# Optimization experiments

Measured on AMD Instinct MI355X. Metric: run time of the kernel, lower is better.

Reference implementation:

```python
import jax, jax.numpy as jnp
import numpy as np

DECAY = 0.99
EPS = 1e-05


def setup_inputs() -> dict:
    key = jax.random.key(0)
    k1, k2, k3, k4 = jax.random.split(key, 4)
    x = jax.random.normal(k1, (32, 64, 64, 64), jnp.float32)          # [B,H,W,dim]
    embed = jax.random.normal(k2, (64, 1024), jnp.float32)            # [dim, n_embed] buffer
    cluster_size = jax.random.uniform(k3, (1024,), jnp.float32)       # EMA cluster-size buffer
    embed_avg = jax.random.normal(k4, (64, 1024), jnp.float32)        # EMA embed-avg buffer
    return {"x": x, "embed": embed, "cluster_size": cluster_size, "embed_avg": embed_avg}


def reference(x, embed, cluster_size, embed_avg):
    dim = x.shape[-1]
    n_embed = embed.shape[1]
    flatten = x.reshape(-1, dim)                                      # [N, dim]
    # squared distances: ||f||^2 - 2 f.E + ||e||^2   -> [N, n_embed]
    dist = ((flatten * flatten).sum(1, keepdims=True)
            - 2.0 * (flatten @ embed)
            + (embed * embed).sum(0, keepdims=True))
    idx = jnp.argmin(dist, axis=1)                                    # [N]
    quantize = jnp.take(embed.T, idx, axis=0).reshape(x.shape)        # codebook gather
    embed_ind = idx.reshape(x.shape[:-1])

    # EMA codebook update (training branch); stats detached as in torch (buffers, .data ops)
    fl = jax.lax.stop_gradient(flatten)
    onehot_sum = jax.ops.segment_sum(jnp.ones_like(idx, dtype=x.dtype), idx, num_segments=n_embed)
    embed_sum = jax.ops.segment_sum(fl, idx, num_segments=n_embed).T  # [dim, n_embed]
    new_cluster_size = DECAY * cluster_size + (1.0 - DECAY) * onehot_sum
    new_embed_avg = DECAY * embed_avg + (1.0 - DECAY) * embed_sum
    n = new_cluster_size.sum()
    cs = (new_cluster_size + EPS) / (n + n_embed * EPS) * n
    new_embed = new_embed_avg / cs[None, :]

    diff = jnp.mean((jax.lax.stop_gradient(quantize) - x) ** 2)       # commitment loss
    quantize_st = x + jax.lax.stop_gradient(quantize - x)             # straight-through
    return (quantize_st, diff, embed_ind, new_cluster_size, new_embed_avg, new_embed)
```

## Files before the change

### kernel.cpp

```cpp
#include <hip/hip_runtime.h>


#define N_ROWS 131072
#define DIM    64
#define NEMB   1024
#define FLAG_CAP 131072
#define TAU 0.02f
#define NRANGE 32

static constexpr float DECAYF = 0.99f;
static constexpr float OMDF   = (float)(1.0 - 0.99);
static constexpr float EPSF   = 1e-5f;
static constexpr float NEPSF  = (float)(1024 * 1e-5);

typedef __attribute__((ext_vector_type(8))) short short8;
typedef __attribute__((ext_vector_type(4))) float f32x4;

static __device__ __forceinline__ unsigned short f2bf(float f) {
    unsigned int u = __builtin_bit_cast(unsigned int, f);
    unsigned int r = (u + 0x7FFFu + ((u >> 16) & 1u)) >> 16;
    return (unsigned short)r;
}
static __device__ __forceinline__ float bf2f(unsigned short h) {
    unsigned int u = ((unsigned int)h) << 16;
    return __builtin_bit_cast(float, u);
}

#define WS_ESUM    0
#define WS_CNTF    65536
#define WS_DIFF    66560
#define WS_FLAGCNT 66561
#define WS_N       66562
#define WS_EE      66564
#define WS_EMBEDT  67588
#define WS_IDX     133124
#define WS_FLAGLST 264196
#define WS_BFRAG   395268
#define WS_CNTPART 460804
#define WS_PART    493572
#define WS_NEED_BYTES ((size_t)(WS_PART + NRANGE * 65536) * 4)

__global__ void prep_kernel(const float* __restrict__ embed,
                            float* __restrict__ embedT,
                            float* __restrict__ ee,
                            uint4* __restrict__ BfragG) {
    int tid = blockIdx.x * 256 + threadIdx.x;
    for (int i = 0; i < 4; ++i) {
        int id = i * 16384 + tid;
        int d = id >> 10, e = id & 1023;
        embedT[e * 64 + d] = embed[id];
    }
    if (tid < NEMB) {
        float s = 0.f;
        for (int d = 0; d < DIM; ++d) {
            float v = embed[d * 1024 + tid];
            s = fmaf(v, v, s);
        }
        ee[tid] = s;
    }
    int fid  = tid >> 6;
    int lane = tid & 63;
    int hl = fid & 1, kt = (fid >> 1) & 1, ct = fid >> 2;
    int col = ct * 16 + (lane & 15);
    int k0  = kt * 32 + (lane >> 4) * 8;
    unsigned short u[8];
    #pragma unroll
    for (int j = 0; j < 8; ++j) {
        float v = -2.0f * embed[(k0 + j) * 1024 + col];
        unsigned short h = f2bf(v);
        if (hl) h = f2bf(v - bf2f(h));
        u[j] = h;
    }
    uint4 wv;
    wv.x = (unsigned)u[0] | ((unsigned)u[1] << 16);
    wv.y = (unsigned)u[2] | ((unsigned)u[3] << 16);
    wv.z = (unsigned)u[4] | ((unsigned)u[5] << 16);
    wv.w = (unsigned)u[6] | ((unsigned)u[7] << 16);
    BfragG[fid * 64 + lane] = wv;
}

__global__ __launch_bounds__(256) void dist_kernel(
        const float* __restrict__ x, const uint4* __restrict__ BfragG,
        const float* __restrict__ ee, const float* __restrict__ embedT,
        float* __restrict__ out_q, float* __restrict__ out_ind,
        int* __restrict__ ws_idx, float* __restrict__ ws_diff,
        int* __restrict__ ws_flagcnt, int* __restrict__ ws_flaglist) {
    __shared__ float sEE[1024];
    __shared__ int   sIdx[64];
    __shared__ float red[4];

    const int t = threadIdx.x;
    const int w = t >> 6, lane = t & 63;
    const int quad = lane >> 4, wl = lane & 15;
    const int rbase = blockIdx.x * 64;

    short8 a_hi[2], a_lo[2];
    {
        int row = rbase + w * 16 + wl;
        #pragma unroll
        for (int kt = 0; kt < 2; ++kt) {
            const float* px = x + (size_t)row * 64 + kt * 32 + quad * 8;
            float4 v0 = *(const float4*)px;
            float4 v1 = *(const float4*)(px + 4);
            float vv[8] = {v0.x, v0.y, v0.z, v0.w, v1.x, v1.y, v1.z, v1.w};
            short8 ah, al;
            #pragma unroll
            for (int j = 0; j < 8; ++j) {
                unsigned short h = f2bf(vv[j]);
                ah[j] = (short)h;
                al[j] = (short)f2bf(vv[j] - bf2f(h));
            }
            a_hi[kt] = ah; a_lo[kt] = al;
        }
    }

    for (int i = t; i < 1024; i += 256) sEE[i] = ee[i];

    float b1[4], b2[4];
    int   i1[4];
    #pragma unroll
    for (int s = 0; s < 4; ++s) { b1[s] = 3.4e38f; b2[s] = 3.4e38f; i1[s] = 0; }

    const f32x4 zacc = {0.f, 0.f, 0.f, 0.f};

    __syncthreads();

    const uint4* bg = BfragG + lane;
    uint4 nb0 = bg[0], nb1 = bg[64], nb2 = bg[128], nb3 = bg[192];
    for (int g = 0; g < 64; ++g) {
        uint4 c_b0 = nb0, c_b1 = nb1, c_b2 = nb2, c_b3 = nb3;
        if (g < 63) {
            const uint4* p = bg + (g + 1) * 256;
            nb0 = p[0]; nb1 = p[64]; nb2 = p[128]; nb3 = p[192];
        }
        short8 bh0 = __builtin_bit_cast(short8, c_b0);
        short8 bl0 = __builtin_bit_cast(short8, c_b1);
        short8 bh1 = __builtin_bit_cast(short8, c_b2);
        short8 bl1 = __builtin_bit_cast(short8, c_b3);
        int col = g * 16 + wl;
        float eec = sEE[col];
        {
            f32x4 c0 = __builtin_amdgcn_mfma_f32_16x16x32_bf16(a_lo[0], bh0, zacc, 0, 0, 0);
            f32x4 c1 = __builtin_amdgcn_mfma_f32_16x16x32_bf16(a_lo[1], bh1, zacc, 0, 0, 0);
            c0 = __builtin_amdgcn_mfma_f32_16x16x32_bf16(a_hi[0], bl0, c0, 0, 0, 0);
            c1 = __builtin_amdgcn_mfma_f32_16x16x32_bf16(a_hi[1], bl1, c1, 0, 0, 0);
            c0 = __builtin_amdgcn_mfma_f32_16x16x32_bf16(a_hi[0], bh0, c0, 0, 0, 0);
            c1 = __builtin_amdgcn_mfma_f32_16x16x32_bf16(a_hi[1], bh1, c1, 0, 0, 0);
            #pragma unroll
            for (int reg = 0; reg < 4; ++reg) {
                float s = c0[reg] + c1[reg] + eec;
                bool lt = s < b1[reg];
                b2[reg] = fminf(fmaxf(s, b1[reg]), b2[reg]);
                i1[reg] = lt ? col : i1[reg];
                b1[reg] = fminf(s, b1[reg]);
            }
        }
    }

    for (int m = 1; m < 16; m <<= 1) {
        #pragma unroll
        for (int s = 0; s < 4; ++s) {
            float ob1 = __shfl_xor(b1[s], m);
            int   oi1 = __shfl_xor(i1[s], m);
            float ob2 = __shfl_xor(b2[s], m);
            if (ob1 < b1[s] || (ob1 == b1[s] && oi1 < i1[s])) {
                b2[s] = fminf(b1[s], ob2); b1[s] = ob1; i1[s] = oi1;
            } else {
                b2[s] = fminf(b2[s], ob1);
            }
        }
    }
    if (wl == 0) {
        #pragma unroll
        for (int s = 0; s < 4; ++s) {
            int rloc = w * 16 + quad * 4 + s;
            int row = rbase + rloc;
            sIdx[rloc] = i1[s];
            ws_idx[row] = i1[s];
            out_ind[row] = (float)i1[s];
            if (b2[s] - b1[s] < TAU) {
                int pos = atomicAdd(ws_flagcnt, 1);
                if (pos < FLAG_CAP) ws_flaglist[pos] = row;
            }
        }
    }
    __syncthreads();

    {
        int r = t >> 2, hh = t & 3;
        int e = sIdx[r];
        const float4* et = (const float4*)(embedT + e * 64 + hh * 16);
        const float4* xr = (const float4*)(x + (size_t)(rbase + r) * 64 + hh * 16);
        float4*       qo = (float4*)(out_q + (size_t)(rbase + r) * 64 + hh * 16);
        float dsum = 0.f;
        #pragma unroll
        for (int v = 0; v < 4; ++v) {
            float4 q4 = et[v];
            float4 x4 = xr[v];
            float dx = q4.x - x4.x, dy = q4.y - x4.y, dz = q4.z - x4.z, dw = q4.w - x4.w;
            float4 o;
            o.x = x4.x + dx; o.y = x4.y + dy; o.z = x4.z + dz; o.w = x4.w + dw;
            qo[v] = o;
            dsum += dx * dx + dy * dy + dz * dz + dw * dw;
        }
        for (int o2 = 32; o2 > 0; o2 >>= 1) dsum += __shfl_down(dsum, o2);
        if (lane == 0) red[w] = dsum;
        __syncthreads();
        if (t == 0) atomicAdd(ws_diff, red[0] + red[1] + red[2] + red[3]);
    }
}

__global__ __launch_bounds__(256) void recheck_kernel(
        const float* __restrict__ x, const float* __restrict__ embed,
        const float* __restrict__ embedT, const float* __restrict__ ee,
        const int* __restrict__ flagcnt, const int* __restrict__ flaglist,
        int* __restrict__ ws_idx, float* __restrict__ out_ind,
        float* __restrict__ out_q, float* __restrict__ ws_diff) {
    __shared__ float sx[8][64];
    __shared__ float sff[8];
    __shared__ int   srow[8];
    __shared__ float sbd[8][256];
    __shared__ int   sbi[8][256];
    const int t = threadIdx.x;
    const int w = t >> 6, lane = t & 63;
    int cnt = *flagcnt;
    if (cnt > FLAG_CAP) cnt = FLAG_CAP;
    int ntiles = (cnt + 7) >> 3;
    for (int tile = blockIdx.x; tile < ntiles; tile += gridDim.x) {
        int base = tile * 8;
        int nr = cnt - base; if (nr > 8) nr = 8;
        __syncthreads();
        if (t < nr) srow[t] = flaglist[base + t];
        __syncthreads();
        for (int l = t; l < nr * 64; l += 256)
            sx[l >> 6][l & 63] = x[(size_t)srow[l >> 6] * 64 + (l & 63)];
        __syncthreads();
        if (t < nr) {
            float ff = 0.f;
            for (int k = 0; k < 64; ++k) ff = fmaf(sx[t][k], sx[t][k], ff);
            sff[t] = ff;
        }
        float acc[8][4];
        #pragma unroll
        for (int r = 0; r < 8; ++r)
            #pragma unroll
            for (int j = 0; j < 4; ++j) acc[r][j] = 0.f;
        int c0 = t * 4;
        for (int k = 0; k < 64; ++k) {
            float4 e4 = *(const float4*)(embed + k * 1024 + c0);
            #pragma unroll
            for (int r = 0; r < 8; ++r) {
                float xk = sx[r][k];
                acc[r][0] = fmaf(xk, e4.x, acc[r][0]);
                acc[r][1] = fmaf(xk, e4.y, acc[r][1]);
                acc[r][2] = fmaf(xk, e4.z, acc[r][2]);
                acc[r][3] = fmaf(xk, e4.w, acc[r][3]);
            }
        }
        __syncthreads();
        #pragma unroll
        for (int r = 0; r < 8; ++r) {
            float ff = sff[r];
            float bd = 3.4e38f; int bi = 0;
            #pragma unroll
            for (int j = 0; j < 4; ++j) {
                float d = (ff - 2.f * acc[r][j]) + ee[c0 + j];
                if (d < bd) { bd = d; bi = c0 + j; }
            }
            sbd[r][t] = bd; sbi[r][t] = bi;
        }
        __syncthreads();
        #pragma unroll
        for (int rr = 0; rr < 2; ++rr) {
            int r = w * 2 + rr;
            if (r < nr) {
                float bd = sbd[r][lane]; int bi = sbi[r][lane];
                #pragma unroll
                for (int k2 = 1; k2 < 4; ++k2) {
                    float od = sbd[r][lane + 64 * k2];
                    int   oi = sbi[r][lane + 64 * k2];
                    if (od < bd || (od == bd && oi < bi)) { bd = od; bi = oi; }
                }
                for (int m = 32; m > 0; m >>= 1) {
                    float od = __shfl_xor(bd, m);
                    int   oi = __shfl_xor(bi, m);
                    if (od < bd || (od == bd && oi < bi)) { bd = od; bi = oi; }
                }
                int row = srow[r];
                int oi_old = ws_idx[row];
                if (bi != oi_old) {
                    float xv = sx[r][lane];
                    float dn   = embedT[bi * 64 + lane] - xv;
                    float dold = embedT[oi_old * 64 + lane] - xv;
                    out_q[(size_t)row * 64 + lane] = xv + dn;
                    float delta = dn * dn - dold * dold;
                    for (int o = 32; o > 0; o >>= 1) delta += __shfl_down(delta, o);
                    if (lane == 0) {
                        ws_idx[row] = bi;
                        out_ind[row] = (float)bi;
                        atomicAdd(ws_diff, delta);
                    }
                }
            }
        }
    }
}

__global__ __launch_bounds__(1024) void scatter_kernel(
        const int* __restrict__ idx, const float* __restrict__ x,
        float* __restrict__ part_or_esum, float* __restrict__ cntp_or_cntf,
        int use_atomic) {
    __shared__ float shist[8192];
    __shared__ float scnt[1024];
    const int t = threadIdx.x;
    const int bid = blockIdx.x;
    const int oct = (bid >> 3) & 7;
    const int rb  = (bid & 7) | ((bid >> 6) << 3);
    const int sid = rb * 8 + oct;
    const int w = t >> 6, lane = t & 63;
    const int g = lane >> 3, d = lane & 7;

    for (int i = t; i < 8192; i += 1024) shist[i] = 0.f;
    if (oct == 0) { if (t < 1024) scnt[t] = 0.f; }
    __syncthreads();

    const int row0 = rb * 4096 + w * 256;
    int rcur = row0 + g;
    int e_n = idx[rcur];
    float x_n = x[(size_t)rcur * 64 + oct * 8 + d];
    for (int it = 0; it < 32; ++it) {
        int e = e_n; float xv = x_n;
        int rnext = rcur + 8;
        if (it < 31) {
            e_n = idx[rnext];
            x_n = x[(size_t)rnext * 64 + oct * 8 + d];
        }
        rcur = rnext;
        atomicAdd(&shist[e * 8 + d], xv);
        if (oct == 0 && d == 0) atomicAdd(&scnt[e], 1.0f);
    }
    __syncthreads();

    if (!use_atomic) {
        float* dst = part_or_esum + (size_t)sid * 8192;
        for (int out = t; out < 8192; out += 1024)
            dst[out] = shist[(out & 1023) * 8 + (out >> 10)];
        if (oct == 0) {
            float* cdst = cntp_or_cntf + rb * 1024;
            if (t < 1024) cdst[t] = scnt[t];
        }
    } else {
        for (int out = t; out < 8192; out += 1024) {
            float v = shist[(out & 1023) * 8 + (out >> 10)];
            if (v != 0.f)
                atomicAdd(&part_or_esum[(oct * 8 + (out >> 10)) * 1024 + (out & 1023)], v);
        }
        if (oct == 0) {
            if (t < 1024) {
                float c = scnt[t];
                if (c != 0.f) atomicAdd(&cntp_or_cntf[t], c);
            }
        }
    }
}

__global__ __launch_bounds__(1024) void finalize1(
        const float* __restrict__ cluster_size, const float* __restrict__ cntp,
        int nrb, const float* __restrict__ ws_diff, float* __restrict__ out_diff,
        float* __restrict__ out_ncs, float* __restrict__ ws_n) {
    int t = threadIdx.x;
    float c = 0.f;
    for (int k = 0; k < nrb; ++k) c += cntp[k * 1024 + t];
    float ncs = DECAYF * cluster_size[t] + OMDF * c;
    out_ncs[t] = ncs;
    __shared__ float sred[16];
    float v = ncs;
    for (int o = 32; o > 0; o >>= 1) v += __shfl_down(v, o);
    if ((t & 63) == 0) sred[t >> 6] = v;
    __syncthreads();
    if (t == 0) {
        float n = 0.f;
        for (int i = 0; i < 16; ++i) n += sred[i];
        ws_n[0] = n;
        out_diff[0] = ws_diff[0] * (1.0f / 8388608.0f);
    }
}

__global__ __launch_bounds__(256) void finalize2(
        const float* __restrict__ embed_avg, const float* __restrict__ part,
        int nrb, const float* __restrict__ out_ncs, const float* __restrict__ ws_n,
        float* __restrict__ out_nea, float* __restrict__ out_ne) {
    int j = blockIdx.x * 256 + threadIdx.x;
    float es = 0.f;
    for (int k = 0; k < nrb; ++k) es += part[(size_t)k * 65536 + j];
    float n = ws_n[0];
    float nea = DECAYF * embed_avg[j] + OMDF * es;
    out_nea[j] = nea;
    float ncs = out_ncs[j & 1023];
    float cs = (ncs + EPSF) / (n + NEPSF) * n;
    out_ne[j] = nea / cs;
}

extern "C" void kernel_launch(void* const* d_in, const int* in_sizes, int n_in,
                              void* d_out, int out_size, void* d_ws, size_t ws_size,
                              hipStream_t stream) {
    const float* x            = (const float*)d_in[0];
    const float* embed        = (const float*)d_in[1];
    const float* cluster_size = (const float*)d_in[2];
    const float* embed_avg    = (const float*)d_in[3];

    float* out = (float*)d_out;
    float* out_q    = out;
    float* out_diff = out + 8388608;
    float* out_ind  = out + 8388609;
    float* out_ncs  = out + 8519681;
    float* out_nea  = out + 8520705;
    float* out_ne   = out + 8586241;

    float* ws = (float*)d_ws;
    float* ws_esum     = ws + WS_ESUM;
    float* ws_cntf     = ws + WS_CNTF;
    float* ws_diff     = ws + WS_DIFF;
    int*   ws_flagcnt  = (int*)(ws + WS_FLAGCNT);
    float* ws_n        = ws + WS_N;
    float* ws_ee       = ws + WS_EE;
    float* ws_embedT   = ws + WS_EMBEDT;
    int*   ws_idx      = (int*)(ws + WS_IDX);
    int*   ws_flaglist = (int*)(ws + WS_FLAGLST);
    uint4* ws_Bfrag    = (uint4*)(ws + WS_BFRAG);
    float* ws_cntpart  = ws + WS_CNTPART;
    float* ws_part     = ws + WS_PART;

    const int use_part = (ws_size >= WS_NEED_BYTES) ? 1 : 0;

    if (use_part) {
        hipMemsetAsync(ws + WS_DIFF, 0, 8, stream);
    } else {
        hipMemsetAsync(d_ws, 0, (size_t)(WS_FLAGCNT + 1) * 4, stream);
    }

    prep_kernel<<<64, 256, 0, stream>>>(embed, ws_embedT, ws_ee, ws_Bfrag);
    dist_kernel<<<N_ROWS / 64, 256, 0, stream>>>(x, ws_Bfrag, ws_ee, ws_embedT,
                                                 out_q, out_ind, ws_idx, ws_diff,
                                                 ws_flagcnt, ws_flaglist);
    recheck_kernel<<<1024, 256, 0, stream>>>(x, embed, ws_embedT, ws_ee,
                                             ws_flagcnt, ws_flaglist,
                                             ws_idx, out_ind, out_q, ws_diff);
    scatter_kernel<<<NRANGE * 8, 1024, 0, stream>>>(
        ws_idx, x,
        use_part ? ws_part : ws_esum,
        use_part ? ws_cntpart : ws_cntf,
        use_part ? 0 : 1);
    finalize1<<<1, 1024, 0, stream>>>(cluster_size,
                                      use_part ? ws_cntpart : ws_cntf,
                                      use_part ? NRANGE : 1,
                                      ws_diff, out_diff, out_ncs, ws_n);
    finalize2<<<256, 256, 0, stream>>>(embed_avg,
                                       use_part ? ws_part : ws_esum,
                                       use_part ? NRANGE : 1,
                                       out_ncs, ws_n, out_nea, out_ne);
}
```

Before: 305.3 us.

## Process four row tiles per wave to reuse codebook fragments across rows

Each wave of the distance kernel now handles 64 rows (four 16-row MFMA tiles) instead of 16, so every codebook B-fragment loaded from global memory feeds four times as many MFMAs. The grid shrinks by four, and blocks start the codebook sweep at a staggered group offset to spread cache traffic. The second-best tracking uses a single med3 instruction, and the recheck kernel handles 16 flagged rows per tile instead of 8. The cost is much higher register pressure (16 tracked rows, 16 A fragments per lane), which may lower occupancy, and only 512 blocks remain to fill the GPU.

```diff
diff --git a/kernel.cpp b/kernel.cpp
--- a/kernel.cpp
+++ b/kernel.cpp
@@ -86,17 +86,18 @@
         int* __restrict__ ws_idx, float* __restrict__ ws_diff,
         int* __restrict__ ws_flagcnt, int* __restrict__ ws_flaglist) {
     __shared__ float sEE[1024];
-    __shared__ int   sIdx[64];
+    __shared__ int   sIdx[256];
     __shared__ float red[4];
 
     const int t = threadIdx.x;
     const int w = t >> 6, lane = t & 63;
     const int quad = lane >> 4, wl = lane & 15;
-    const int rbase = blockIdx.x * 64;
-
-    short8 a_hi[2], a_lo[2];
-    {
-        int row = rbase + w * 16 + wl;
+    const int rbase = blockIdx.x * 256;
+
+    short8 a_hi[4][2], a_lo[4][2];
+    #pragma unroll
+    for (int rt = 0; rt < 4; ++rt) {
+        int row = rbase + w * 64 + rt * 16 + wl;
         #pragma unroll
         for (int kt = 0; kt < 2; ++kt) {
             const float* px = x + (size_t)row * 64 + kt * 32 + quad * 8;
@@ -110,56 +111,63 @@
                 ah[j] = (short)h;
                 al[j] = (short)f2bf(vv[j] - bf2f(h));
             }
-            a_hi[kt] = ah; a_lo[kt] = al;
+            a_hi[rt][kt] = ah; a_lo[rt][kt] = al;
         }
     }
 
     for (int i = t; i < 1024; i += 256) sEE[i] = ee[i];
 
-    float b1[4], b2[4];
-    int   i1[4];
+    float b1[16], b2[16];
+    int   i1[16];
     #pragma unroll
-    for (int s = 0; s < 4; ++s) { b1[s] = 3.4e38f; b2[s] = 3.4e38f; i1[s] = 0; }
+    for (int s = 0; s < 16; ++s) { b1[s] = 3.4e38f; b2[s] = 3.4e38f; i1[s] = 0; }
 
     const f32x4 zacc = {0.f, 0.f, 0.f, 0.f};
 
     __syncthreads();
 
-    const uint4* bg = BfragG + lane;
-    uint4 nb0 = bg[0], nb1 = bg[64], nb2 = bg[128], nb3 = bg[192];
+    const int goff = blockIdx.x & 63;
+    int gv = goff;
+    {
+    }
+    const uint4* p0 = BfragG + gv * 256 + lane;
+    uint4 nb0 = p0[0], nb1 = p0[64], nb2 = p0[128], nb3 = p0[192];
     for (int g = 0; g < 64; ++g) {
         uint4 c_b0 = nb0, c_b1 = nb1, c_b2 = nb2, c_b3 = nb3;
+        const int col = gv * 16 + wl;
         if (g < 63) {
-            const uint4* p = bg + (g + 1) * 256;
+            gv = (gv + 1) & 63;
+            const uint4* p = BfragG + gv * 256 + lane;
             nb0 = p[0]; nb1 = p[64]; nb2 = p[128]; nb3 = p[192];
         }
         short8 bh0 = __builtin_bit_cast(short8, c_b0);
         short8 bl0 = __builtin_bit_cast(short8, c_b1);
         short8 bh1 = __builtin_bit_cast(short8, c_b2);
         short8 bl1 = __builtin_bit_cast(short8, c_b3);
-        int col = g * 16 + wl;
         float eec = sEE[col];
-        {
-            f32x4 c0 = __builtin_amdgcn_mfma_f32_16x16x32_bf16(a_lo[0], bh0, zacc, 0, 0, 0);
-            f32x4 c1 = __builtin_amdgcn_mfma_f32_16x16x32_bf16(a_lo[1], bh1, zacc, 0, 0, 0);
-            c0 = __builtin_amdgcn_mfma_f32_16x16x32_bf16(a_hi[0], bl0, c0, 0, 0, 0);
-            c1 = __builtin_amdgcn_mfma_f32_16x16x32_bf16(a_hi[1], bl1, c1, 0, 0, 0);
-            c0 = __builtin_amdgcn_mfma_f32_16x16x32_bf16(a_hi[0], bh0, c0, 0, 0, 0);
-            c1 = __builtin_amdgcn_mfma_f32_16x16x32_bf16(a_hi[1], bh1, c1, 0, 0, 0);
+        #pragma unroll
+        for (int rt = 0; rt < 4; ++rt) {
+            f32x4 c0 = __builtin_amdgcn_mfma_f32_16x16x32_bf16(a_lo[rt][0], bh0, zacc, 0, 0, 0);
+            f32x4 c1 = __builtin_amdgcn_mfma_f32_16x16x32_bf16(a_lo[rt][1], bh1, zacc, 0, 0, 0);
+            c0 = __builtin_amdgcn_mfma_f32_16x16x32_bf16(a_hi[rt][0], bl0, c0, 0, 0, 0);
+            c1 = __builtin_amdgcn_mfma_f32_16x16x32_bf16(a_hi[rt][1], bl1, c1, 0, 0, 0);
+            c0 = __builtin_amdgcn_mfma_f32_16x16x32_bf16(a_hi[rt][0], bh0, c0, 0, 0, 0);
+            c1 = __builtin_amdgcn_mfma_f32_16x16x32_bf16(a_hi[rt][1], bh1, c1, 0, 0, 0);
             #pragma unroll
             for (int reg = 0; reg < 4; ++reg) {
                 float s = c0[reg] + c1[reg] + eec;
-                bool lt = s < b1[reg];
-                b2[reg] = fminf(fmaxf(s, b1[reg]), b2[reg]);
-                i1[reg] = lt ? col : i1[reg];
-                b1[reg] = fminf(s, b1[reg]);
+                int st = rt * 4 + reg;
+                bool lt = s < b1[st];
+                b2[st] = __builtin_amdgcn_fmed3f(s, b1[st], b2[st]);
+                i1[st] = lt ? col : i1[st];
+                b1[st] = fminf(s, b1[st]);
             }
         }
     }
 
     for (int m = 1; m < 16; m <<= 1) {
         #pragma unroll
-        for (int s = 0; s < 4; ++s) {
+        for (int s = 0; s < 16; ++s) {
             float ob1 = __shfl_xor(b1[s], m);
             int   oi1 = __shfl_xor(i1[s], m);
             float ob2 = __shfl_xor(b2[s], m);
@@ -172,8 +180,9 @@
     }
     if (wl == 0) {
         #pragma unroll
-        for (int s = 0; s < 4; ++s) {
-            int rloc = w * 16 + quad * 4 + s;
+        for (int s = 0; s < 16; ++s) {
+            int rt = s >> 2, reg = s & 3;
+            int rloc = w * 64 + rt * 16 + quad * 4 + reg;
             int row = rbase + rloc;
             sIdx[rloc] = i1[s];
             ws_idx[row] = i1[s];
@@ -187,21 +196,24 @@
     __syncthreads();
 
     {
-        int r = t >> 2, hh = t & 3;
-        int e = sIdx[r];
-        const float4* et = (const float4*)(embedT + e * 64 + hh * 16);
-        const float4* xr = (const float4*)(x + (size_t)(rbase + r) * 64 + hh * 16);
-        float4*       qo = (float4*)(out_q + (size_t)(rbase + r) * 64 + hh * 16);
         float dsum = 0.f;
         #pragma unroll
-        for (int v = 0; v < 4; ++v) {
-            float4 q4 = et[v];
-            float4 x4 = xr[v];
-            float dx = q4.x - x4.x, dy = q4.y - x4.y, dz = q4.z - x4.z, dw = q4.w - x4.w;
-            float4 o;
-            o.x = x4.x + dx; o.y = x4.y + dy; o.z = x4.z + dz; o.w = x4.w + dw;
-            qo[v] = o;
-            dsum += dx * dx + dy * dy + dz * dz + dw * dw;
+        for (int half = 0; half < 2; ++half) {
+            int r = half * 128 + (t >> 1), hh = t & 1;
+            int e = sIdx[r];
+            const float4* et = (const float4*)(embedT + e * 64 + hh * 32);
+            const float4* xr = (const float4*)(x + (size_t)(rbase + r) * 64 + hh * 32);
+            float4*       qo = (float4*)(out_q + (size_t)(rbase + r) * 64 + hh * 32);
+            #pragma unroll
+            for (int v = 0; v < 8; ++v) {
+                float4 q4 = et[v];
+                float4 x4 = xr[v];
+                float dx = q4.x - x4.x, dy = q4.y - x4.y, dz = q4.z - x4.z, dw = q4.w - x4.w;
+                float4 o;
+                o.x = x4.x + dx; o.y = x4.y + dy; o.z = x4.z + dz; o.w = x4.w + dw;
+                qo[v] = o;
+                dsum += dx * dx + dy * dy + dz * dz + dw * dw;
+            }
         }
         for (int o2 = 32; o2 > 0; o2 >>= 1) dsum += __shfl_down(dsum, o2);
         if (lane == 0) red[w] = dsum;
@@ -216,19 +228,19 @@
         const int* __restrict__ flagcnt, const int* __restrict__ flaglist,
         int* __restrict__ ws_idx, float* __restrict__ out_ind,
         float* __restrict__ out_q, float* __restrict__ ws_diff) {
-    __shared__ float sx[8][64];
-    __shared__ float sff[8];
-    __shared__ int   srow[8];
-    __shared__ float sbd[8][256];
-    __shared__ int   sbi[8][256];
+    __shared__ float sx[16][64];
+    __shared__ float sff[16];
+    __shared__ int   srow[16];
+    __shared__ float sbd[16][256];
+    __shared__ int   sbi[16][256];
     const int t = threadIdx.x;
     const int w = t >> 6, lane = t & 63;
     int cnt = *flagcnt;
     if (cnt > FLAG_CAP) cnt = FLAG_CAP;
-    int ntiles = (cnt + 7) >> 3;
+    int ntiles = (cnt + 15) >> 4;
     for (int tile = blockIdx.x; tile < ntiles; tile += gridDim.x) {
-        int base = tile * 8;
-        int nr = cnt - base; if (nr > 8) nr = 8;
+        int base = tile * 16;
+        int nr = cnt - base; if (nr > 16) nr = 16;
         __syncthreads();
         if (t < nr) srow[t] = flaglist[base + t];
         __syncthreads();
@@ -240,16 +252,16 @@
             for (int k = 0; k < 64; ++k) ff = fmaf(sx[t][k], sx[t][k], ff);
             sff[t] = ff;
         }
-        float acc[8][4];
-        #pragma unroll
-        for (int r = 0; r < 8; ++r)
+        float acc[16][4];
+        #pragma unroll
+        for (int r = 0; r < 16; ++r)
             #pragma unroll
             for (int j = 0; j < 4; ++j) acc[r][j] = 0.f;
         int c0 = t * 4;
         for (int k = 0; k < 64; ++k) {
             float4 e4 = *(const float4*)(embed + k * 1024 + c0);
             #pragma unroll
-            for (int r = 0; r < 8; ++r) {
+            for (int r = 0; r < 16; ++r) {
                 float xk = sx[r][k];
                 acc[r][0] = fmaf(xk, e4.x, acc[r][0]);
                 acc[r][1] = fmaf(xk, e4.y, acc[r][1]);
@@ -259,20 +271,22 @@
         }
         __syncthreads();
         #pragma unroll
-        for (int r = 0; r < 8; ++r) {
-            float ff = sff[r];
-            float bd = 3.4e38f; int bi = 0;
-            #pragma unroll
-            for (int j = 0; j < 4; ++j) {
-                float d = (ff - 2.f * acc[r][j]) + ee[c0 + j];
-                if (d < bd) { bd = d; bi = c0 + j; }
-            }
-            sbd[r][t] = bd; sbi[r][t] = bi;
-        }
-        __syncthreads();
-        #pragma unroll
-        for (int rr = 0; rr < 2; ++rr) {
-            int r = w * 2 + rr;
+        for (int r = 0; r < 16; ++r) {
+            if (r < nr) {
+                float ff = sff[r];
+                float bd = 3.4e38f; int bi = 0;
+                #pragma unroll
+                for (int j = 0; j < 4; ++j) {
+                    float d = (ff - 2.f * acc[r][j]) + ee[c0 + j];
+                    if (d < bd) { bd = d; bi = c0 + j; }
+                }
+                sbd[r][t] = bd; sbi[r][t] = bi;
+            }
+        }
+        __syncthreads();
+        #pragma unroll
+        for (int rr = 0; rr < 4; ++rr) {
+            int r = w * 4 + rr;
             if (r < nr) {
                 float bd = sbd[r][lane]; int bi = sbi[r][lane];
                 #pragma unroll
@@ -440,9 +454,9 @@
     }
 
     prep_kernel<<<64, 256, 0, stream>>>(embed, ws_embedT, ws_ee, ws_Bfrag);
-    dist_kernel<<<N_ROWS / 64, 256, 0, stream>>>(x, ws_Bfrag, ws_ee, ws_embedT,
-                                                 out_q, out_ind, ws_idx, ws_diff,
-                                                 ws_flagcnt, ws_flaglist);
+    dist_kernel<<<N_ROWS / 256, 256, 0, stream>>>(x, ws_Bfrag, ws_ee, ws_embedT,
+                                                  out_q, out_ind, ws_idx, ws_diff,
+                                                  ws_flagcnt, ws_flaglist);
     recheck_kernel<<<1024, 256, 0, stream>>>(x, embed, ws_embedT, ws_ee,
                                              ws_flagcnt, ws_flaglist,
                                              ws_idx, out_ind, out_q, ws_diff);
```

Measured after the change: 268.3 us. -12.1%, faster.

## Fuse recheck into dist kernel, pack index into distance key, merge finalizers

Applied to the files above, without the earlier changes.

The distance kernel now handles 128 rows per block with two row tiles that share each codebook fragment load. It packs the codebook index into the low mantissa bits of the distance, so top-2 tracking becomes fmin/fmed3 with no index select. Near-tie rows are queued in shared memory and re-scored exactly in fp32 inside the same kernel, which removes the separate recheck launch and the global flag atomics. The two finalize kernels are merged into one, and the memset is replaced by a zero write in prep. Truncating the mantissa lowers key precision, so the tie threshold is widened to compensate, which can send more rows through the slow exact path. Each block also starts at a different codebook offset to spread the fragment reads.

```diff
diff --git a/kernel.cpp b/kernel.cpp
--- a/kernel.cpp
+++ b/kernel.cpp
@@ -4,9 +4,9 @@
 #define N_ROWS 131072
 #define DIM    64
 #define NEMB   1024
-#define FLAG_CAP 131072
-#define TAU 0.02f
 #define NRANGE 32
+#define KMASK  0xFFFFFC00u
+#define TAUK   0.15f
 
 static constexpr float DECAYF = 0.99f;
 static constexpr float OMDF   = (float)(1.0 - 0.99);
@@ -43,8 +43,10 @@
 __global__ void prep_kernel(const float* __restrict__ embed,
                             float* __restrict__ embedT,
                             float* __restrict__ ee,
-                            uint4* __restrict__ BfragG) {
+                            uint4* __restrict__ BfragG,
+                            float* __restrict__ ws_diff) {
     int tid = blockIdx.x * 256 + threadIdx.x;
+    if (tid == 0) ws_diff[0] = 0.f;
     for (int i = 0; i < 4; ++i) {
         int id = i * 16384 + tid;
         int d = id >> 10, e = id & 1023;
@@ -81,22 +83,30 @@
 
 __global__ __launch_bounds__(256) void dist_kernel(
         const float* __restrict__ x, const uint4* __restrict__ BfragG,
-        const float* __restrict__ ee, const float* __restrict__ embedT,
+        const float* __restrict__ ee, const float* __restrict__ embed,
+        const float* __restrict__ embedT,
         float* __restrict__ out_q, float* __restrict__ out_ind,
-        int* __restrict__ ws_idx, float* __restrict__ ws_diff,
-        int* __restrict__ ws_flagcnt, int* __restrict__ ws_flaglist) {
+        int* __restrict__ ws_idx, float* __restrict__ ws_diff) {
     __shared__ float sEE[1024];
-    __shared__ int   sIdx[64];
+    __shared__ int   sIdx[128];
     __shared__ float red[4];
+    __shared__ int   sFlagCnt;
+    __shared__ int   sFlagRows[128];
+    __shared__ float sx[8][64];
+    __shared__ float sff[8];
+    __shared__ float sbdw[8][4];
+    __shared__ int   sbiw[8][4];
+    __shared__ int   schg[8];
 
     const int t = threadIdx.x;
     const int w = t >> 6, lane = t & 63;
     const int quad = lane >> 4, wl = lane & 15;
-    const int rbase = blockIdx.x * 64;
-
-    short8 a_hi[2], a_lo[2];
-    {
-        int row = rbase + w * 16 + wl;
+    const int rbase = blockIdx.x * 128;
+
+    short8 a_hi[2][2], a_lo[2][2];
+    #pragma unroll
+    for (int rt = 0; rt < 2; ++rt) {
+        int row = rbase + w * 32 + rt * 16 + wl;
         #pragma unroll
         for (int kt = 0; kt < 2; ++kt) {
             const float* px = x + (size_t)row * 64 + kt * 32 + quad * 8;
@@ -110,91 +120,115 @@
                 ah[j] = (short)h;
                 al[j] = (short)f2bf(vv[j] - bf2f(h));
             }
-            a_hi[kt] = ah; a_lo[kt] = al;
+            a_hi[rt][kt] = ah; a_lo[rt][kt] = al;
         }
     }
 
     for (int i = t; i < 1024; i += 256) sEE[i] = ee[i];
-
-    float b1[4], b2[4];
-    int   i1[4];
+    if (t == 0) sFlagCnt = 0;
+
+    float b1[8], b2[8];
     #pragma unroll
-    for (int s = 0; s < 4; ++s) { b1[s] = 3.4e38f; b2[s] = 3.4e38f; i1[s] = 0; }
+    for (int s = 0; s < 8; ++s) { b1[s] = 3.4e38f; b2[s] = 3.4e38f; }
 
     const f32x4 zacc = {0.f, 0.f, 0.f, 0.f};
 
     __syncthreads();
 
-    const uint4* bg = BfragG + lane;
-    uint4 nb0 = bg[0], nb1 = bg[64], nb2 = bg[128], nb3 = bg[192];
-    for (int g = 0; g < 64; ++g) {
-        uint4 c_b0 = nb0, c_b1 = nb1, c_b2 = nb2, c_b3 = nb3;
-        if (g < 63) {
-            const uint4* p = bg + (g + 1) * 256;
-            nb0 = p[0]; nb1 = p[64]; nb2 = p[128]; nb3 = p[192];
-        }
-        short8 bh0 = __builtin_bit_cast(short8, c_b0);
-        short8 bl0 = __builtin_bit_cast(short8, c_b1);
-        short8 bh1 = __builtin_bit_cast(short8, c_b2);
-        short8 bl1 = __builtin_bit_cast(short8, c_b3);
-        int col = g * 16 + wl;
-        float eec = sEE[col];
-        {
-            f32x4 c0 = __builtin_amdgcn_mfma_f32_16x16x32_bf16(a_lo[0], bh0, zacc, 0, 0, 0);
-            f32x4 c1 = __builtin_amdgcn_mfma_f32_16x16x32_bf16(a_lo[1], bh1, zacc, 0, 0, 0);
-            c0 = __builtin_amdgcn_mfma_f32_16x16x32_bf16(a_hi[0], bl0, c0, 0, 0, 0);
-            c1 = __builtin_amdgcn_mfma_f32_16x16x32_bf16(a_hi[1], bl1, c1, 0, 0, 0);
-            c0 = __builtin_amdgcn_mfma_f32_16x16x32_bf16(a_hi[0], bh0, c0, 0, 0, 0);
-            c1 = __builtin_amdgcn_mfma_f32_16x16x32_bf16(a_hi[1], bh1, c1, 0, 0, 0);
-            #pragma unroll
-            for (int reg = 0; reg < 4; ++reg) {
-                float s = c0[reg] + c1[reg] + eec;
-                bool lt = s < b1[reg];
-                b2[reg] = fminf(fmaxf(s, b1[reg]), b2[reg]);
-                i1[reg] = lt ? col : i1[reg];
-                b1[reg] = fminf(s, b1[reg]);
-            }
-        }
-    }
+    const int goff = blockIdx.x & 63;
+
+#define GBODY(CB0, CB1, CB2, CB3, COLV)                                        \
+    {                                                                          \
+        short8 bh0 = __builtin_bit_cast(short8, CB0);                          \
+        short8 bl0 = __builtin_bit_cast(short8, CB1);                          \
+        short8 bh1 = __builtin_bit_cast(short8, CB2);                          \
+        short8 bl1 = __builtin_bit_cast(short8, CB3);                          \
+        float eec = sEE[COLV];                                                 \
+        unsigned colu = (unsigned)(COLV);                                      \
+        _Pragma("unroll")                                                      \
+        for (int rt = 0; rt < 2; ++rt) {                                       \
+            f32x4 c0 = __builtin_amdgcn_mfma_f32_16x16x32_bf16(a_lo[rt][0], bh0, zacc, 0, 0, 0); \
+            f32x4 c1 = __builtin_amdgcn_mfma_f32_16x16x32_bf16(a_lo[rt][1], bh1, zacc, 0, 0, 0); \
+            c0 = __builtin_amdgcn_mfma_f32_16x16x32_bf16(a_hi[rt][0], bl0, c0, 0, 0, 0); \
+            c1 = __builtin_amdgcn_mfma_f32_16x16x32_bf16(a_hi[rt][1], bl1, c1, 0, 0, 0); \
+            c0 = __builtin_amdgcn_mfma_f32_16x16x32_bf16(a_hi[rt][0], bh0, c0, 0, 0, 0); \
+            c1 = __builtin_amdgcn_mfma_f32_16x16x32_bf16(a_hi[rt][1], bh1, c1, 0, 0, 0); \
+            _Pragma("unroll")                                                  \
+            for (int reg = 0; reg < 4; ++reg) {                                \
+                float s = c0[reg] + c1[reg] + eec;                             \
+                unsigned ku = (__builtin_bit_cast(unsigned, s) & KMASK) | colu;\
+                float key = __builtin_bit_cast(float, ku);                     \
+                int st = rt * 4 + reg;                                         \
+                b2[st] = __builtin_amdgcn_fmed3f(key, b1[st], b2[st]);         \
+                b1[st] = fminf(key, b1[st]);                                   \
+            }                                                                  \
+        }                                                                      \
+    }
+
+    {
+        const uint4* bgl = BfragG + lane;
+        int gA = goff, gB = (goff + 1) & 63;
+        const uint4* pA = bgl + gA * 256;
+        uint4 A0 = pA[0], A1 = pA[64], A2 = pA[128], A3 = pA[192];
+        const uint4* pB = bgl + gB * 256;
+        uint4 B0 = pB[0], B1 = pB[64], B2 = pB[128], B3 = pB[192];
+        for (int it = 0; it < 64; it += 2) {
+            int colA = ((goff + it) & 63) * 16 + wl;
+            GBODY(A0, A1, A2, A3, colA);
+            if (it + 2 < 64) {
+                const uint4* p = bgl + (((goff + it + 2) & 63) * 256);
+                A0 = p[0]; A1 = p[64]; A2 = p[128]; A3 = p[192];
+            }
+            int colB = ((goff + it + 1) & 63) * 16 + wl;
+            GBODY(B0, B1, B2, B3, colB);
+            if (it + 3 < 64) {
+                const uint4* p = bgl + (((goff + it + 3) & 63) * 256);
+                B0 = p[0]; B1 = p[64]; B2 = p[128]; B3 = p[192];
+            }
+        }
+    }
+#undef GBODY
 
     for (int m = 1; m < 16; m <<= 1) {
         #pragma unroll
-        for (int s = 0; s < 4; ++s) {
-            float ob1 = __shfl_xor(b1[s], m);
-            int   oi1 = __shfl_xor(i1[s], m);
-            float ob2 = __shfl_xor(b2[s], m);
-            if (ob1 < b1[s] || (ob1 == b1[s] && oi1 < i1[s])) {
-                b2[s] = fminf(b1[s], ob2); b1[s] = ob1; i1[s] = oi1;
-            } else {
-                b2[s] = fminf(b2[s], ob1);
-            }
+        for (int s = 0; s < 8; ++s) {
+            float o1 = __shfl_xor(b1[s], m);
+            float o2 = __shfl_xor(b2[s], m);
+            float mx = fmaxf(b1[s], o1);
+            b1[s] = fminf(b1[s], o1);
+            b2[s] = fminf(fminf(b2[s], o2), mx);
         }
     }
     if (wl == 0) {
         #pragma unroll
-        for (int s = 0; s < 4; ++s) {
-            int rloc = w * 16 + quad * 4 + s;
+        for (int s = 0; s < 8; ++s) {
+            int rt = s >> 2, reg = s & 3;
+            int rloc = w * 32 + rt * 16 + quad * 4 + reg;
             int row = rbase + rloc;
-            sIdx[rloc] = i1[s];
-            ws_idx[row] = i1[s];
-            out_ind[row] = (float)i1[s];
-            if (b2[s] - b1[s] < TAU) {
-                int pos = atomicAdd(ws_flagcnt, 1);
-                if (pos < FLAG_CAP) ws_flaglist[pos] = row;
+            unsigned kb = __builtin_bit_cast(unsigned, b1[s]);
+            int col = (int)(kb & 1023u);
+            sIdx[rloc] = col;
+            ws_idx[row] = col;
+            out_ind[row] = (float)col;
+            float v1 = __builtin_bit_cast(float, kb & KMASK);
+            float v2 = __builtin_bit_cast(float, __builtin_bit_cast(unsigned, b2[s]) & KMASK);
+            if (v2 - v1 < TAUK) {
+                int p = atomicAdd(&sFlagCnt, 1);
+                sFlagRows[p] = rloc;
             }
         }
     }
     __syncthreads();
 
     {
-        int r = t >> 2, hh = t & 3;
+        int r = t >> 1, hh = t & 1;
         int e = sIdx[r];
-        const float4* et = (const float4*)(embedT + e * 64 + hh * 16);
-        const float4* xr = (const float4*)(x + (size_t)(rbase + r) * 64 + hh * 16);
-        float4*       qo = (float4*)(out_q + (size_t)(rbase + r) * 64 + hh * 16);
+        const float4* et = (const float4*)(embedT + e * 64 + hh * 32);
+        const float4* xr = (const float4*)(x + (size_t)(rbase + r) * 64 + hh * 32);
+        float4*       qo = (float4*)(out_q + (size_t)(rbase + r) * 64 + hh * 32);
         float dsum = 0.f;
         #pragma unroll
-        for (int v = 0; v < 4; ++v) {
+        for (int v = 0; v < 8; ++v) {
             float4 q4 = et[v];
             float4 x4 = xr[v];
             float dx = q4.x - x4.x, dy = q4.y - x4.y, dz = q4.z - x4.z, dw = q4.w - x4.w;
@@ -208,32 +242,16 @@
         __syncthreads();
         if (t == 0) atomicAdd(ws_diff, red[0] + red[1] + red[2] + red[3]);
     }
-}
-
-__global__ __launch_bounds__(256) void recheck_kernel(
-        const float* __restrict__ x, const float* __restrict__ embed,
-        const float* __restrict__ embedT, const float* __restrict__ ee,
-        const int* __restrict__ flagcnt, const int* __restrict__ flaglist,
-        int* __restrict__ ws_idx, float* __restrict__ out_ind,
-        float* __restrict__ out_q, float* __restrict__ ws_diff) {
-    __shared__ float sx[8][64];
-    __shared__ float sff[8];
-    __shared__ int   srow[8];
-    __shared__ float sbd[8][256];
-    __shared__ int   sbi[8][256];
-    const int t = threadIdx.x;
-    const int w = t >> 6, lane = t & 63;
-    int cnt = *flagcnt;
-    if (cnt > FLAG_CAP) cnt = FLAG_CAP;
-    int ntiles = (cnt + 7) >> 3;
-    for (int tile = blockIdx.x; tile < ntiles; tile += gridDim.x) {
-        int base = tile * 8;
-        int nr = cnt - base; if (nr > 8) nr = 8;
-        __syncthreads();
-        if (t < nr) srow[t] = flaglist[base + t];
-        __syncthreads();
-        for (int l = t; l < nr * 64; l += 256)
-            sx[l >> 6][l & 63] = x[(size_t)srow[l >> 6] * 64 + (l & 63)];
+
+    __syncthreads();
+    int fcnt = sFlagCnt;
+    for (int base = 0; base < fcnt; base += 8) {
+        int nr = fcnt - base; if (nr > 8) nr = 8;
+        __syncthreads();
+        for (int l = t; l < nr * 64; l += 256) {
+            int rl = sFlagRows[base + (l >> 6)];
+            sx[l >> 6][l & 63] = x[(size_t)(rbase + rl) * 64 + (l & 63)];
+        }
         __syncthreads();
         if (t < nr) {
             float ff = 0.f;
@@ -245,9 +263,9 @@
         for (int r = 0; r < 8; ++r)
             #pragma unroll
             for (int j = 0; j < 4; ++j) acc[r][j] = 0.f;
-        int c0 = t * 4;
+        int c0i = t * 4;
         for (int k = 0; k < 64; ++k) {
-            float4 e4 = *(const float4*)(embed + k * 1024 + c0);
+            float4 e4 = *(const float4*)(embed + k * 1024 + c0i);
             #pragma unroll
             for (int r = 0; r < 8; ++r) {
                 float xk = sx[r][k];
@@ -260,47 +278,52 @@
         __syncthreads();
         #pragma unroll
         for (int r = 0; r < 8; ++r) {
-            float ff = sff[r];
-            float bd = 3.4e38f; int bi = 0;
-            #pragma unroll
-            for (int j = 0; j < 4; ++j) {
-                float d = (ff - 2.f * acc[r][j]) + ee[c0 + j];
-                if (d < bd) { bd = d; bi = c0 + j; }
-            }
-            sbd[r][t] = bd; sbi[r][t] = bi;
-        }
-        __syncthreads();
-        #pragma unroll
-        for (int rr = 0; rr < 2; ++rr) {
-            int r = w * 2 + rr;
             if (r < nr) {
-                float bd = sbd[r][lane]; int bi = sbi[r][lane];
+                float ff = sff[r];
+                float bd = 3.4e38f; int bi = 0;
                 #pragma unroll
-                for (int k2 = 1; k2 < 4; ++k2) {
-                    float od = sbd[r][lane + 64 * k2];
-                    int   oi = sbi[r][lane + 64 * k2];
-                    if (od < bd || (od == bd && oi < bi)) { bd = od; bi = oi; }
+                for (int j = 0; j < 4; ++j) {
+                    float d = (ff - 2.f * acc[r][j]) + sEE[c0i + j];
+                    if (d < bd) { bd = d; bi = c0i + j; }
                 }
                 for (int m = 32; m > 0; m >>= 1) {
                     float od = __shfl_xor(bd, m);
                     int   oi = __shfl_xor(bi, m);
                     if (od < bd || (od == bd && oi < bi)) { bd = od; bi = oi; }
                 }
-                int row = srow[r];
-                int oi_old = ws_idx[row];
-                if (bi != oi_old) {
-                    float xv = sx[r][lane];
-                    float dn   = embedT[bi * 64 + lane] - xv;
-                    float dold = embedT[oi_old * 64 + lane] - xv;
-                    out_q[(size_t)row * 64 + lane] = xv + dn;
-                    float delta = dn * dn - dold * dold;
-                    for (int o = 32; o > 0; o >>= 1) delta += __shfl_down(delta, o);
-                    if (lane == 0) {
-                        ws_idx[row] = bi;
-                        out_ind[row] = (float)bi;
-                        atomicAdd(ws_diff, delta);
-                    }
-                }
+                if (lane == 0) { sbdw[r][w] = bd; sbiw[r][w] = bi; }
+            }
+        }
+        __syncthreads();
+        if (t < nr) {
+            float bd = sbdw[t][0]; int bi = sbiw[t][0];
+            #pragma unroll
+            for (int k2 = 1; k2 < 4; ++k2) {
+                float od = sbdw[t][k2]; int oi = sbiw[t][k2];
+                if (od < bd || (od == bd && oi < bi)) { bd = od; bi = oi; }
+            }
+            int rl = sFlagRows[base + t];
+            int oi_ = sIdx[rl];
+            schg[t] = (bi != oi_) ? bi : -1;
+            if (bi != oi_) {
+                ws_idx[rbase + rl] = bi;
+                out_ind[rbase + rl] = (float)bi;
+            }
+        }
+        __syncthreads();
+        for (int r = w; r < nr; r += 4) {
+            int ni = schg[r];
+            if (ni >= 0) {
+                int rl = sFlagRows[base + r];
+                int row = rbase + rl;
+                int oi_ = sIdx[rl];
+                float xv = sx[r][lane];
+                float dn   = embedT[ni * 64 + lane] - xv;
+                float dold = embedT[oi_ * 64 + lane] - xv;
+                out_q[(size_t)row * 64 + lane] = xv + dn;
+                float delta = dn * dn - dold * dold;
+                for (int o = 32; o > 0; o >>= 1) delta += __shfl_down(delta, o);
+                if (lane == 0) atomicAdd(ws_diff, delta);
             }
         }
     }
@@ -364,39 +387,37 @@
     }
 }
 
-__global__ __launch_bounds__(1024) void finalize1(
+__global__ __launch_bounds__(1024) void finalizeF(
         const float* __restrict__ cluster_size, const float* __restrict__ cntp,
-        int nrb, const float* __restrict__ ws_diff, float* __restrict__ out_diff,
-        float* __restrict__ out_ncs, float* __restrict__ ws_n) {
-    int t = threadIdx.x;
+        const float* __restrict__ part, int nrb,
+        const float* __restrict__ ws_diff, const float* __restrict__ embed_avg,
+        float* __restrict__ out_diff, float* __restrict__ out_ncs,
+        float* __restrict__ out_nea, float* __restrict__ out_ne) {
+    __shared__ float sred[16];
+    __shared__ float sn;
+    const int tid = threadIdx.x;
+    const int b = blockIdx.x;
     float c = 0.f;
-    for (int k = 0; k < nrb; ++k) c += cntp[k * 1024 + t];
-    float ncs = DECAYF * cluster_size[t] + OMDF * c;
-    out_ncs[t] = ncs;
-    __shared__ float sred[16];
+    for (int k = 0; k < nrb; ++k) c += cntp[k * 1024 + tid];
+    float ncs = DECAYF * cluster_size[tid] + OMDF * c;
     float v = ncs;
     for (int o = 32; o > 0; o >>= 1) v += __shfl_down(v, o);
-    if ((t & 63) == 0) sred[t >> 6] = v;
-    __syncthreads();
-    if (t == 0) {
+    if ((tid & 63) == 0) sred[tid >> 6] = v;
+    __syncthreads();
+    if (tid == 0) {
         float n = 0.f;
         for (int i = 0; i < 16; ++i) n += sred[i];
-        ws_n[0] = n;
-        out_diff[0] = ws_diff[0] * (1.0f / 8388608.0f);
-    }
-}
-
-__global__ __launch_bounds__(256) void finalize2(
-        const float* __restrict__ embed_avg, const float* __restrict__ part,
-        int nrb, const float* __restrict__ out_ncs, const float* __restrict__ ws_n,
-        float* __restrict__ out_nea, float* __restrict__ out_ne) {
-    int j = blockIdx.x * 256 + threadIdx.x;
+        sn = n;
+        if (b == 0) out_diff[0] = ws_diff[0] * (1.0f / 8388608.0f);
+    }
+    __syncthreads();
+    float n = sn;
+    if (b == 0) out_ncs[tid] = ncs;
+    int j = b * 1024 + tid;
     float es = 0.f;
     for (int k = 0; k < nrb; ++k) es += part[(size_t)k * 65536 + j];
-    float n = ws_n[0];
     float nea = DECAYF * embed_avg[j] + OMDF * es;
     out_nea[j] = nea;
-    float ncs = out_ncs[j & 1023];
     float cs = (ncs + EPSF) / (n + NEPSF) * n;
     out_ne[j] = nea / cs;
 }
@@ -421,42 +442,32 @@
     float* ws_esum     = ws + WS_ESUM;
     float* ws_cntf     = ws + WS_CNTF;
     float* ws_diff     = ws + WS_DIFF;
-    int*   ws_flagcnt  = (int*)(ws + WS_FLAGCNT);
-    float* ws_n        = ws + WS_N;
     float* ws_ee       = ws + WS_EE;
     float* ws_embedT   = ws + WS_EMBEDT;
     int*   ws_idx      = (int*)(ws + WS_IDX);
-    int*   ws_flaglist = (int*)(ws + WS_FLAGLST);
     uint4* ws_Bfrag    = (uint4*)(ws + WS_BFRAG);
     float* ws_cntpart  = ws + WS_CNTPART;
     float* ws_part     = ws + WS_PART;
 
     const int use_part = (ws_size >= WS_NEED_BYTES) ? 1 : 0;
 
-    if (use_part) {
-        hipMemsetAsync(ws + WS_DIFF, 0, 8, stream);
-    } else {
+    if (!use_part) {
         hipMemsetAsync(d_ws, 0, (size_t)(WS_FLAGCNT + 1) * 4, stream);
     }
 
-    prep_kernel<<<64, 256, 0, stream>>>(embed, ws_embedT, ws_ee, ws_Bfrag);
-    dist_kernel<<<N_ROWS / 64, 256, 0, stream>>>(x, ws_Bfrag, ws_ee, ws_embedT,
-                                                 out_q, out_ind, ws_idx, ws_diff,
-                                                 ws_flagcnt, ws_flaglist);
-    recheck_kernel<<<1024, 256, 0, stream>>>(x, embed, ws_embedT, ws_ee,
-                                             ws_flagcnt, ws_flaglist,
-                                             ws_idx, out_ind, out_q, ws_diff);
+    prep_kernel<<<64, 256, 0, stream>>>(embed, ws_embedT, ws_ee, ws_Bfrag, ws_diff);
+    dist_kernel<<<N_ROWS / 128, 256, 0, stream>>>(x, ws_Bfrag, ws_ee, embed,
+                                                  ws_embedT, out_q, out_ind,
+                                                  ws_idx, ws_diff);
     scatter_kernel<<<NRANGE * 8, 1024, 0, stream>>>(
         ws_idx, x,
         use_part ? ws_part : ws_esum,
         use_part ? ws_cntpart : ws_cntf,
         use_part ? 0 : 1);
-    finalize1<<<1, 1024, 0, stream>>>(cluster_size,
-                                      use_part ? ws_cntpart : ws_cntf,
-                                      use_part ? NRANGE : 1,
-                                      ws_diff, out_diff, out_ncs, ws_n);
-    finalize2<<<256, 256, 0, stream>>>(embed_avg,
+    finalizeF<<<64, 1024, 0, stream>>>(cluster_size,
+                                       use_part ? ws_cntpart : ws_cntf,
                                        use_part ? ws_part : ws_esum,
                                        use_part ? NRANGE : 1,
-                                       out_ncs, ws_n, out_nea, out_ne);
-}
+                                       ws_diff, embed_avg,
+                                       out_diff, out_ncs, out_nea, out_ne);
+}
```

Result: faster. 257.1 us (-15.8%).
